# Optimization experiments

Hardware: AMD Instinct MI355X
Metric: run time of the kernel (lower is better)

## Reference

```python
import jax, jax.numpy as jnp
import numpy as np

N_NODES = 100000
N_EDGES = 3200000


def _spmm(edge_index, edge_vals, support):
    # adj @ support where adj is COO: out[r] += v * support[c]
    msgs = support[edge_index[1]] * edge_vals[:, None]  # [E, F]
    return jax.ops.segment_sum(msgs, edge_index[0], num_segments=N_NODES)


def _gcn(x, edge_index, edge_vals, W, b):
    support = x @ W
    return _spmm(edge_index, edge_vals, support) + b


def setup_inputs() -> dict:
    key = jax.random.key(0)
    ks = jax.random.split(key, 10)
    nhid1, nhid2, nout = 256, 128, 128
    x = jax.random.normal(ks[0], (N_NODES, nhid1), dtype=jnp.float32)
    edge_index = jax.random.randint(ks[1], (2, N_EDGES), 0, N_NODES, dtype=jnp.int32)
    edge_vals = jax.random.uniform(ks[2], (N_EDGES,), dtype=jnp.float32)
    def init_w(k, fan_in, fan_out):
        stdv = 1.0 / np.sqrt(fan_out)
        return jax.random.uniform(k, (fan_in, fan_out), minval=-stdv, maxval=stdv, dtype=jnp.float32)
    def init_b(k, fan_out):
        stdv = 1.0 / np.sqrt(fan_out)
        return jax.random.uniform(k, (fan_out,), minval=-stdv, maxval=stdv, dtype=jnp.float32)
    return {
        "x": x, "edge_index": edge_index, "edge_vals": edge_vals,
        "W1": init_w(ks[3], nhid1, nhid2), "b1": init_b(ks[4], nhid2),
        "W2": init_w(ks[5], nhid2, nout), "b2": init_b(ks[6], nout),
        "W3": init_w(ks[7], nout, nout), "b3": init_b(ks[8], nout),
    }


def reference(x, edge_index, edge_vals, W1, b1, W2, b2, W3, b3):
    TIMEPOINTS = 4
    # eval mode: dropout is identity
    h = jax.nn.relu(_gcn(x, edge_index, edge_vals, W1, b1))
    h = jax.nn.relu(_gcn(h, edge_index, edge_vals, W2, b2))
    preds = [h]
    for _ in range(1, TIMEPOINTS):
        h = jax.nn.relu(_gcn(h, edge_index, edge_vals, W3, b3))
        preds.append(h)
    return jnp.stack(preds, axis=0)  # [T, N, noutSR]
```

## Files before the change

### kernel.cpp

```cpp
#include <hip/hip_runtime.h>

#define NNODES 100000
#define NEDGES 3200000
#define NF 128
#define SCAN_CHUNK 512
#define NCHUNK 196
#define SC_BLOCKS_PER_GRP 384

typedef short bf16x8 __attribute__((ext_vector_type(8)));
typedef short s16x4 __attribute__((ext_vector_type(4)));
typedef short s16x8 __attribute__((ext_vector_type(8)));
typedef float f32x4 __attribute__((ext_vector_type(4)));

__device__ inline unsigned short f2bf(float f) {
    union { float f; unsigned int u; } v; v.f = f;
    unsigned int u = v.u;
    unsigned int r = (u + 0x7fffu + ((u >> 16) & 1u)) >> 16;
    return (unsigned short)r;
}
__device__ inline float bf_lo(unsigned int u) { return __uint_as_float(u << 16); }
__device__ inline float bf_hi(unsigned int u) { return __uint_as_float(u & 0xffff0000u); }


__global__ void hist_rank_kernel(const int* __restrict__ rows, int* __restrict__ counts,
                                 int* __restrict__ rank) {
    int e = blockIdx.x * 256 + threadIdx.x;
    if (e < NEDGES) rank[e] = atomicAdd(&counts[rows[e]], 1);
}

__global__ void chunk_sum_kernel(const int* __restrict__ counts, int* __restrict__ partial) {
    __shared__ int sdata[4];
    int t = threadIdx.x;
    int base = blockIdx.x * SCAN_CHUNK;
    int s = 0;
    int i0 = base + t;        if (i0 < NNODES) s += counts[i0];
    int i1 = base + t + 256;  if (i1 < NNODES) s += counts[i1];
    #pragma unroll
    for (int off = 32; off > 0; off >>= 1) s += __shfl_down(s, off, 64);
    if ((t & 63) == 0) sdata[t >> 6] = s;
    __syncthreads();
    if (t == 0) partial[blockIdx.x] = sdata[0] + sdata[1] + sdata[2] + sdata[3];
}

__global__ void scan_partials_kernel(const int* __restrict__ partial, int* __restrict__ chunk_off) {
    __shared__ int tmp[256];
    int t = threadIdx.x;
    int v = (t < NCHUNK) ? partial[t] : 0;
    tmp[t] = v;
    __syncthreads();
    #pragma unroll
    for (int off = 1; off < 256; off <<= 1) {
        int u = (t >= off) ? tmp[t - off] : 0;
        __syncthreads();
        tmp[t] += u;
        __syncthreads();
    }
    if (t < NCHUNK) chunk_off[t] = tmp[t] - v;
}

__global__ void scan_chunks_kernel(const int* __restrict__ counts,
                                   const int* __restrict__ chunk_off,
                                   int* __restrict__ rowptr) {
    __shared__ int tmp[SCAN_CHUNK];
    int t = threadIdx.x;
    int i = blockIdx.x * SCAN_CHUNK + t;
    int v = (i < NNODES) ? counts[i] : 0;
    tmp[t] = v;
    __syncthreads();
    #pragma unroll
    for (int off = 1; off < SCAN_CHUNK; off <<= 1) {
        int u = (t >= off) ? tmp[t - off] : 0;
        __syncthreads();
        tmp[t] += u;
        __syncthreads();
    }
    if (i < NNODES) rowptr[i] = chunk_off[blockIdx.x] + tmp[t] - v;
    if (i == 0) rowptr[NNODES] = NEDGES;
}

__global__ __launch_bounds__(256) void scatter8_kernel(const int* __restrict__ rows,
                                                       const int* __restrict__ cols,
                                                       const float* __restrict__ vals,
                                                       const int* __restrict__ rowptr,
                                                       const int* __restrict__ rank,
                                                       unsigned int* __restrict__ csr_p) {
    int grp = blockIdx.x & 7;
    int blk = blockIdx.x >> 3;
    int lo = grp * 12500;
    int hi = lo + 12500;
    for (int e = blk * 256 + threadIdx.x; e < NEDGES; e += SC_BLOCKS_PER_GRP * 256) {
        int r = rows[e];
        if (r >= lo && r < hi) {
            unsigned int q = (unsigned int)__float2int_rn(vals[e] * 32768.0f);
            q = q > 32767u ? 32767u : q;
            csr_p[rowptr[r] + rank[e]] = ((unsigned int)cols[e] << 15) | q;
        }
    }
}


template <int K>
__global__ __launch_bounds__(256) void gemm_bf16_kernel(const float* __restrict__ A,
                                                        const float* __restrict__ W,
                                                        unsigned short* __restrict__ Csup,
                                                        int M) {
    __shared__ short SL[18432];
    short* As = SL;
    short* Wt = SL + 128 * 72;

    int tid = threadIdx.x;
    int w = tid >> 6, l = tid & 63;
    int g = l >> 4, r16 = l & 15;
    int m0 = blockIdx.x * 128;

    f32x4 zero = {0.f, 0.f, 0.f, 0.f};
    f32x4 acc[2][8];
    #pragma unroll
    for (int i = 0; i < 2; ++i)
        #pragma unroll
        for (int j = 0; j < 8; ++j) acc[i][j] = zero;

    for (int k0 = 0; k0 < K; k0 += 64) {
        #pragma unroll
        for (int j = 0; j < 8; ++j) {
            int f = tid + j * 256;
            int row = f >> 4, kq = f & 15;
            int gr = m0 + row;
            float4 v = make_float4(0.f, 0.f, 0.f, 0.f);
            if (gr < M) v = *reinterpret_cast<const float4*>(&A[(size_t)gr * K + k0 + kq * 4]);
            s16x4 p;
            p[0] = (short)f2bf(v.x); p[1] = (short)f2bf(v.y);
            p[2] = (short)f2bf(v.z); p[3] = (short)f2bf(v.w);
            *reinterpret_cast<s16x4*>(&As[row * 72 + kq * 4]) = p;
        }
        #pragma unroll
        for (int j = 0; j < 8; ++j) {
            int f = tid + j * 256;
            int wr = f >> 5, cq = f & 31;
            float4 v = *reinterpret_cast<const float4*>(&W[(size_t)(k0 + wr) * 128 + cq * 4]);
            Wt[(cq * 4 + 0) * 72 + wr] = (short)f2bf(v.x);
            Wt[(cq * 4 + 1) * 72 + wr] = (short)f2bf(v.y);
            Wt[(cq * 4 + 2) * 72 + wr] = (short)f2bf(v.z);
            Wt[(cq * 4 + 3) * 72 + wr] = (short)f2bf(v.w);
        }
        __syncthreads();
        #pragma unroll
        for (int kc = 0; kc < 64; kc += 32) {
            bf16x8 a0 = *reinterpret_cast<const bf16x8*>(&As[(w * 32 + r16) * 72 + kc + g * 8]);
            bf16x8 a1 = *reinterpret_cast<const bf16x8*>(&As[(w * 32 + 16 + r16) * 72 + kc + g * 8]);
            bf16x8 b[8];
            #pragma unroll
            for (int cf = 0; cf < 8; ++cf)
                b[cf] = *reinterpret_cast<const bf16x8*>(&Wt[(cf * 16 + r16) * 72 + kc + g * 8]);
            #pragma unroll
            for (int cf = 0; cf < 8; ++cf) {
                acc[0][cf] = __builtin_amdgcn_mfma_f32_16x16x32_bf16(a0, b[cf], acc[0][cf], 0, 0, 0);
                acc[1][cf] = __builtin_amdgcn_mfma_f32_16x16x32_bf16(a1, b[cf], acc[1][cf], 0, 0, 0);
            }
        }
        __syncthreads();
    }

    short* Csw = SL + w * (32 * 136);
    #pragma unroll
    for (int fi = 0; fi < 2; ++fi)
        #pragma unroll
        for (int cf = 0; cf < 8; ++cf)
            #pragma unroll
            for (int reg = 0; reg < 4; ++reg) {
                int rowl = fi * 16 + g * 4 + reg;
                Csw[rowl * 136 + cf * 16 + r16] = (short)f2bf(acc[fi][cf][reg]);
            }
    __syncthreads();
    #pragma unroll
    for (int it = 0; it < 8; ++it) {
        int rowl = g + it * 4;
        int grow = m0 + w * 32 + rowl;
        if (grow < M)
            *reinterpret_cast<s16x8*>(&Csup[(size_t)grow * 128 + r16 * 8]) =
                *reinterpret_cast<const s16x8*>(&Csw[rowl * 136 + r16 * 8]);
    }
}


__global__ __launch_bounds__(256) void spmm_bf16_kernel(const int* __restrict__ rowptr,
                                                        const unsigned int* __restrict__ csr_p,
                                                        const unsigned int* __restrict__ sup,
                                                        const float* __restrict__ bias,
                                                        float* __restrict__ out) {
    int wave = threadIdx.x >> 6;
    int lane = threadIdx.x & 63;
    int r = blockIdx.x * 4 + wave;
    int start = rowptr[r], end = rowptr[r + 1];
    const float SCL = 1.0f / 32768.0f;

    float a0x = 0.f, a0y = 0.f, a1x = 0.f, a1y = 0.f;
    float a2x = 0.f, a2y = 0.f, a3x = 0.f, a3y = 0.f;
    int e = start;
    for (; e + 3 < end; e += 4) {
        unsigned int p0 = csr_p[e];
        unsigned int p1 = csr_p[e + 1];
        unsigned int p2 = csr_p[e + 2];
        unsigned int p3 = csr_p[e + 3];
        unsigned int u0 = sup[(size_t)(p0 >> 15) * 64 + lane];
        unsigned int u1 = sup[(size_t)(p1 >> 15) * 64 + lane];
        unsigned int u2 = sup[(size_t)(p2 >> 15) * 64 + lane];
        unsigned int u3 = sup[(size_t)(p3 >> 15) * 64 + lane];
        float v0 = (float)(p0 & 0x7fffu) * SCL;
        float v1 = (float)(p1 & 0x7fffu) * SCL;
        float v2 = (float)(p2 & 0x7fffu) * SCL;
        float v3 = (float)(p3 & 0x7fffu) * SCL;
        a0x += v0 * bf_lo(u0); a0y += v0 * bf_hi(u0);
        a1x += v1 * bf_lo(u1); a1y += v1 * bf_hi(u1);
        a2x += v2 * bf_lo(u2); a2y += v2 * bf_hi(u2);
        a3x += v3 * bf_lo(u3); a3y += v3 * bf_hi(u3);
    }
    for (; e < end; ++e) {
        unsigned int p = csr_p[e];
        unsigned int u = sup[(size_t)(p >> 15) * 64 + lane];
        float v = (float)(p & 0x7fffu) * SCL;
        a0x += v * bf_lo(u); a0y += v * bf_hi(u);
    }
    float2 b2 = reinterpret_cast<const float2*>(bias)[lane];
    float2 o;
    o.x = fmaxf(a0x + a1x + a2x + a3x + b2.x, 0.f);
    o.y = fmaxf(a0y + a1y + a2y + a3y + b2.y, 0.f);
    reinterpret_cast<float2*>(out)[(size_t)r * 64 + lane] = o;
}


extern "C" void kernel_launch(void* const* d_in, const int* in_sizes, int n_in,
                              void* d_out, int out_size, void* d_ws, size_t ws_size,
                              hipStream_t stream) {
    const float* x     = (const float*)d_in[0];
    const int*   eidx  = (const int*)d_in[1];
    const float* evals = (const float*)d_in[2];
    const float* W1    = (const float*)d_in[3];
    const float* b1    = (const float*)d_in[4];
    const float* W2    = (const float*)d_in[5];
    const float* b2    = (const float*)d_in[6];
    const float* W3    = (const float*)d_in[7];
    const float* b3    = (const float*)d_in[8];
    float* out = (float*)d_out;

    const int* e_rows = eidx;
    const int* e_cols = eidx + NEDGES;

    char* ws = (char*)d_ws;
    size_t off = 0;
    auto alloc = [&](size_t bytes) -> void* {
        void* p = ws + off;
        off += (bytes + 255) & ~(size_t)255;
        return p;
    };
    int*            counts    = (int*)alloc((size_t)NNODES * 4);
    int*            rowptr    = (int*)alloc((size_t)(NNODES + 1) * 4);
    int*            partial   = (int*)alloc(256 * 4);
    int*            chunk_off = (int*)alloc(256 * 4);
    int*            rank      = (int*)alloc((size_t)NEDGES * 4);
    unsigned int*   csr_p     = (unsigned int*)alloc((size_t)NEDGES * 4);
    unsigned short* supportA  = (unsigned short*)alloc((size_t)NNODES * NF * 2);

    const size_t SL_ = (size_t)NNODES * NF;
    float* h1 = out + 3 * SL_;

    hipMemsetAsync(counts, 0, (size_t)NNODES * 4, stream);
    hist_rank_kernel<<<NEDGES / 256, 256, 0, stream>>>(e_rows, counts, rank);
    chunk_sum_kernel<<<NCHUNK, 256, 0, stream>>>(counts, partial);
    scan_partials_kernel<<<1, 256, 0, stream>>>(partial, chunk_off);
    scan_chunks_kernel<<<NCHUNK, SCAN_CHUNK, 0, stream>>>(counts, chunk_off, rowptr);
    scatter8_kernel<<<8 * SC_BLOCKS_PER_GRP, 256, 0, stream>>>(e_rows, e_cols, evals, rowptr,
                                                               rank, csr_p);

    const int gemm_grid = (NNODES + 127) / 128;
    const int spmm_grid = NNODES / 4;
    const unsigned int* supU = (const unsigned int*)supportA;

    gemm_bf16_kernel<256><<<gemm_grid, 256, 0, stream>>>(x, W1, supportA, NNODES);
    spmm_bf16_kernel<<<spmm_grid, 256, 0, stream>>>(rowptr, csr_p, supU, b1, h1);
    gemm_bf16_kernel<128><<<gemm_grid, 256, 0, stream>>>(h1, W2, supportA, NNODES);
    spmm_bf16_kernel<<<spmm_grid, 256, 0, stream>>>(rowptr, csr_p, supU, b2, out);
    gemm_bf16_kernel<128><<<gemm_grid, 256, 0, stream>>>(out, W3, supportA, NNODES);
    spmm_bf16_kernel<<<spmm_grid, 256, 0, stream>>>(rowptr, csr_p, supU, b3, out + SL_);
    gemm_bf16_kernel<128><<<gemm_grid, 256, 0, stream>>>(out + SL_, W3, supportA, NNODES);
    spmm_bf16_kernel<<<spmm_grid, 256, 0, stream>>>(rowptr, csr_p, supU, b3, out + 2 * SL_);
    gemm_bf16_kernel<128><<<gemm_grid, 256, 0, stream>>>(out + 2 * SL_, W3, supportA, NNODES);
    spmm_bf16_kernel<<<spmm_grid, 256, 0, stream>>>(rowptr, csr_p, supU, b3, out + 3 * SL_);
}
```

Measured before the change: 1.281 ms.

## Sort CSR edges by column tile within rows and use persistent SpMM grid

The CSR build now keys edges by (row, column-tile of 8192 nodes), so within each row the neighbors are grouped by column range. A 2048-block SpMM grid, with waves striding through rows, then processes the same column tile at roughly the same time across the GPU, which should improve L2 locality of the support gathers. In exchange the counts, scan and rowptr arrays grow sixteenfold and preprocessing has more scan work. The SpMM also switches from one-row-per-wave launches to a grid-stride loop.

```diff
diff --git a/kernel.cpp b/kernel.cpp
--- a/kernel.cpp
+++ b/kernel.cpp
@@ -3,8 +3,10 @@
 #define NNODES 100000
 #define NEDGES 3200000
 #define NF 128
-#define SCAN_CHUNK 512
-#define NCHUNK 196
+#define COLSH 13
+#define NTILE 16
+#define NKEYS (NNODES * NTILE)
+#define NCHUNK16 3125
 #define SC_BLOCKS_PER_GRP 384
 
 typedef short bf16x8 __attribute__((ext_vector_type(8)));
@@ -22,19 +24,20 @@
 __device__ inline float bf_hi(unsigned int u) { return __uint_as_float(u & 0xffff0000u); }
 
 
-__global__ void hist_rank_kernel(const int* __restrict__ rows, int* __restrict__ counts,
-                                 int* __restrict__ rank) {
+__global__ void hist_rank_kernel(const int* __restrict__ rows, const int* __restrict__ cols,
+                                 int* __restrict__ counts, int* __restrict__ rank) {
     int e = blockIdx.x * 256 + threadIdx.x;
-    if (e < NEDGES) rank[e] = atomicAdd(&counts[rows[e]], 1);
+    if (e < NEDGES) {
+        int key = (rows[e] << 4) | (cols[e] >> COLSH);
+        rank[e] = atomicAdd(&counts[key], 1);
+    }
 }
 
 __global__ void chunk_sum_kernel(const int* __restrict__ counts, int* __restrict__ partial) {
     __shared__ int sdata[4];
     int t = threadIdx.x;
-    int base = blockIdx.x * SCAN_CHUNK;
-    int s = 0;
-    int i0 = base + t;        if (i0 < NNODES) s += counts[i0];
-    int i1 = base + t + 256;  if (i1 < NNODES) s += counts[i1];
+    int base = blockIdx.x * 512;
+    int s = counts[base + t] + counts[base + t + 256];
     #pragma unroll
     for (int off = 32; off > 0; off >>= 1) s += __shfl_down(s, off, 64);
     if ((t & 63) == 0) sdata[t >> 6] = s;
@@ -43,39 +46,52 @@
 }
 
 __global__ void scan_partials_kernel(const int* __restrict__ partial, int* __restrict__ chunk_off) {
-    __shared__ int tmp[256];
+    __shared__ int tsum[512];
     int t = threadIdx.x;
-    int v = (t < NCHUNK) ? partial[t] : 0;
-    tmp[t] = v;
+    int loc[7];
+    int s = 0;
+    #pragma unroll
+    for (int i = 0; i < 7; ++i) {
+        int idx = t * 7 + i;
+        int v = (idx < NCHUNK16) ? partial[idx] : 0;
+        loc[i] = s;
+        s += v;
+    }
+    tsum[t] = s;
     __syncthreads();
     #pragma unroll
-    for (int off = 1; off < 256; off <<= 1) {
-        int u = (t >= off) ? tmp[t - off] : 0;
-        __syncthreads();
-        tmp[t] += u;
-        __syncthreads();
-    }
-    if (t < NCHUNK) chunk_off[t] = tmp[t] - v;
+    for (int off = 1; off < 512; off <<= 1) {
+        int u = (t >= off) ? tsum[t - off] : 0;
+        __syncthreads();
+        tsum[t] += u;
+        __syncthreads();
+    }
+    int base = (t > 0) ? tsum[t - 1] : 0;
+    #pragma unroll
+    for (int i = 0; i < 7; ++i) {
+        int idx = t * 7 + i;
+        if (idx < NCHUNK16) chunk_off[idx] = base + loc[i];
+    }
 }
 
 __global__ void scan_chunks_kernel(const int* __restrict__ counts,
                                    const int* __restrict__ chunk_off,
                                    int* __restrict__ rowptr) {
-    __shared__ int tmp[SCAN_CHUNK];
+    __shared__ int tmp[512];
     int t = threadIdx.x;
-    int i = blockIdx.x * SCAN_CHUNK + t;
-    int v = (i < NNODES) ? counts[i] : 0;
+    int i = blockIdx.x * 512 + t;
+    int v = counts[i];
     tmp[t] = v;
     __syncthreads();
     #pragma unroll
-    for (int off = 1; off < SCAN_CHUNK; off <<= 1) {
+    for (int off = 1; off < 512; off <<= 1) {
         int u = (t >= off) ? tmp[t - off] : 0;
         __syncthreads();
         tmp[t] += u;
         __syncthreads();
     }
-    if (i < NNODES) rowptr[i] = chunk_off[blockIdx.x] + tmp[t] - v;
-    if (i == 0) rowptr[NNODES] = NEDGES;
+    rowptr[i] = chunk_off[blockIdx.x] + tmp[t] - v;
+    if (i == 0) rowptr[NKEYS] = NEDGES;
 }
 
 __global__ __launch_bounds__(256) void scatter8_kernel(const int* __restrict__ rows,
@@ -91,9 +107,11 @@
     for (int e = blk * 256 + threadIdx.x; e < NEDGES; e += SC_BLOCKS_PER_GRP * 256) {
         int r = rows[e];
         if (r >= lo && r < hi) {
+            int c = cols[e];
             unsigned int q = (unsigned int)__float2int_rn(vals[e] * 32768.0f);
             q = q > 32767u ? 32767u : q;
-            csr_p[rowptr[r] + rank[e]] = ((unsigned int)cols[e] << 15) | q;
+            int key = (r << 4) | (c >> COLSH);
+            csr_p[rowptr[key] + rank[e]] = ((unsigned int)c << 15) | q;
         }
     }
 }
@@ -190,42 +208,44 @@
                                                         float* __restrict__ out) {
     int wave = threadIdx.x >> 6;
     int lane = threadIdx.x & 63;
-    int r = blockIdx.x * 4 + wave;
-    int start = rowptr[r], end = rowptr[r + 1];
     const float SCL = 1.0f / 32768.0f;
-
-    float a0x = 0.f, a0y = 0.f, a1x = 0.f, a1y = 0.f;
-    float a2x = 0.f, a2y = 0.f, a3x = 0.f, a3y = 0.f;
-    int e = start;
-    for (; e + 3 < end; e += 4) {
-        unsigned int p0 = csr_p[e];
-        unsigned int p1 = csr_p[e + 1];
-        unsigned int p2 = csr_p[e + 2];
-        unsigned int p3 = csr_p[e + 3];
-        unsigned int u0 = sup[(size_t)(p0 >> 15) * 64 + lane];
-        unsigned int u1 = sup[(size_t)(p1 >> 15) * 64 + lane];
-        unsigned int u2 = sup[(size_t)(p2 >> 15) * 64 + lane];
-        unsigned int u3 = sup[(size_t)(p3 >> 15) * 64 + lane];
-        float v0 = (float)(p0 & 0x7fffu) * SCL;
-        float v1 = (float)(p1 & 0x7fffu) * SCL;
-        float v2 = (float)(p2 & 0x7fffu) * SCL;
-        float v3 = (float)(p3 & 0x7fffu) * SCL;
-        a0x += v0 * bf_lo(u0); a0y += v0 * bf_hi(u0);
-        a1x += v1 * bf_lo(u1); a1y += v1 * bf_hi(u1);
-        a2x += v2 * bf_lo(u2); a2y += v2 * bf_hi(u2);
-        a3x += v3 * bf_lo(u3); a3y += v3 * bf_hi(u3);
-    }
-    for (; e < end; ++e) {
-        unsigned int p = csr_p[e];
-        unsigned int u = sup[(size_t)(p >> 15) * 64 + lane];
-        float v = (float)(p & 0x7fffu) * SCL;
-        a0x += v * bf_lo(u); a0y += v * bf_hi(u);
-    }
     float2 b2 = reinterpret_cast<const float2*>(bias)[lane];
-    float2 o;
-    o.x = fmaxf(a0x + a1x + a2x + a3x + b2.x, 0.f);
-    o.y = fmaxf(a0y + a1y + a2y + a3y + b2.y, 0.f);
-    reinterpret_cast<float2*>(out)[(size_t)r * 64 + lane] = o;
+
+    for (int r = blockIdx.x * 4 + wave; r < NNODES; r += 8192) {
+        int start = rowptr[r << 4], end = rowptr[(r + 1) << 4];
+
+        float a0x = 0.f, a0y = 0.f, a1x = 0.f, a1y = 0.f;
+        float a2x = 0.f, a2y = 0.f, a3x = 0.f, a3y = 0.f;
+        int e = start;
+        for (; e + 3 < end; e += 4) {
+            unsigned int p0 = csr_p[e];
+            unsigned int p1 = csr_p[e + 1];
+            unsigned int p2 = csr_p[e + 2];
+            unsigned int p3 = csr_p[e + 3];
+            unsigned int u0 = sup[(size_t)(p0 >> 15) * 64 + lane];
+            unsigned int u1 = sup[(size_t)(p1 >> 15) * 64 + lane];
+            unsigned int u2 = sup[(size_t)(p2 >> 15) * 64 + lane];
+            unsigned int u3 = sup[(size_t)(p3 >> 15) * 64 + lane];
+            float v0 = (float)(p0 & 0x7fffu) * SCL;
+            float v1 = (float)(p1 & 0x7fffu) * SCL;
+            float v2 = (float)(p2 & 0x7fffu) * SCL;
+            float v3 = (float)(p3 & 0x7fffu) * SCL;
+            a0x += v0 * bf_lo(u0); a0y += v0 * bf_hi(u0);
+            a1x += v1 * bf_lo(u1); a1y += v1 * bf_hi(u1);
+            a2x += v2 * bf_lo(u2); a2y += v2 * bf_hi(u2);
+            a3x += v3 * bf_lo(u3); a3y += v3 * bf_hi(u3);
+        }
+        for (; e < end; ++e) {
+            unsigned int p = csr_p[e];
+            unsigned int u = sup[(size_t)(p >> 15) * 64 + lane];
+            float v = (float)(p & 0x7fffu) * SCL;
+            a0x += v * bf_lo(u); a0y += v * bf_hi(u);
+        }
+        float2 o;
+        o.x = fmaxf(a0x + a1x + a2x + a3x + b2.x, 0.f);
+        o.y = fmaxf(a0y + a1y + a2y + a3y + b2.y, 0.f);
+        reinterpret_cast<float2*>(out)[(size_t)r * 64 + lane] = o;
+    }
 }
 
 
@@ -253,10 +273,10 @@
         off += (bytes + 255) & ~(size_t)255;
         return p;
     };
-    int*            counts    = (int*)alloc((size_t)NNODES * 4);
-    int*            rowptr    = (int*)alloc((size_t)(NNODES + 1) * 4);
-    int*            partial   = (int*)alloc(256 * 4);
-    int*            chunk_off = (int*)alloc(256 * 4);
+    int*            counts    = (int*)alloc((size_t)NKEYS * 4);
+    int*            rowptr    = (int*)alloc((size_t)(NKEYS + 1) * 4);
+    int*            partial   = (int*)alloc((size_t)NCHUNK16 * 4);
+    int*            chunk_off = (int*)alloc((size_t)NCHUNK16 * 4);
     int*            rank      = (int*)alloc((size_t)NEDGES * 4);
     unsigned int*   csr_p     = (unsigned int*)alloc((size_t)NEDGES * 4);
     unsigned short* supportA  = (unsigned short*)alloc((size_t)NNODES * NF * 2);
@@ -264,16 +284,16 @@
     const size_t SL_ = (size_t)NNODES * NF;
     float* h1 = out + 3 * SL_;
 
-    hipMemsetAsync(counts, 0, (size_t)NNODES * 4, stream);
-    hist_rank_kernel<<<NEDGES / 256, 256, 0, stream>>>(e_rows, counts, rank);
-    chunk_sum_kernel<<<NCHUNK, 256, 0, stream>>>(counts, partial);
-    scan_partials_kernel<<<1, 256, 0, stream>>>(partial, chunk_off);
-    scan_chunks_kernel<<<NCHUNK, SCAN_CHUNK, 0, stream>>>(counts, chunk_off, rowptr);
+    hipMemsetAsync(counts, 0, (size_t)NKEYS * 4, stream);
+    hist_rank_kernel<<<NEDGES / 256, 256, 0, stream>>>(e_rows, e_cols, counts, rank);
+    chunk_sum_kernel<<<NCHUNK16, 256, 0, stream>>>(counts, partial);
+    scan_partials_kernel<<<1, 512, 0, stream>>>(partial, chunk_off);
+    scan_chunks_kernel<<<NCHUNK16, 512, 0, stream>>>(counts, chunk_off, rowptr);
     scatter8_kernel<<<8 * SC_BLOCKS_PER_GRP, 256, 0, stream>>>(e_rows, e_cols, evals, rowptr,
                                                                rank, csr_p);
 
     const int gemm_grid = (NNODES + 127) / 128;
-    const int spmm_grid = NNODES / 4;
+    const int spmm_grid = 2048;
     const unsigned int* supU = (const unsigned int*)supportA;
 
     gemm_bf16_kernel<256><<<gemm_grid, 256, 0, stream>>>(x, W1, supportA, NNODES);
```

Result: no change. 1.303 ms (+1.7%).
